# Kernel tuning notes

Measured on AMD Instinct MI355X. Metric: run time of the kernel, lower is better.

The kernel has to match this reference:

```python
import jax, jax.numpy as jnp
import numpy as np

N, EM, EW, L, S = 20000, 100000, 25000, 128, 6


def _mlp(x, W1, b1, W2, b2, g, beta):
    # Linear -> ReLU -> Linear -> LayerNorm
    h = jax.nn.relu(x @ W1 + b1) @ W2 + b2
    mu = jnp.mean(h, axis=-1, keepdims=True)
    var = jnp.mean((h - mu) ** 2, axis=-1, keepdims=True)
    return g * (h - mu) * jax.lax.rsqrt(var + 1e-5) + beta


def _scatter_mean(attr, recv, n):
    s = jax.ops.segment_sum(attr, recv, num_segments=n)
    c = jax.ops.segment_sum(jnp.ones((attr.shape[0], 1), attr.dtype), recv, num_segments=n)
    return s / jnp.maximum(c, 1.0)


def setup_inputs() -> dict:
    key = jax.random.key(0)
    ks = jax.random.split(key, 16)

    def w(k, shape, fan_in):
        return (jax.random.normal(k, shape, jnp.float32) / np.sqrt(fan_in).astype(np.float32))

    inp = {
        'x': jax.random.normal(ks[0], (N, L), jnp.float32),
        'mesh_edge_attr': jax.random.normal(ks[1], (EM, L), jnp.float32),
        'world_edge_attr': jax.random.normal(ks[2], (EW, L), jnp.float32),
        'mesh_edge_index': jax.random.randint(ks[3], (2, EM), 0, N),
        'world_edge_index': jax.random.randint(ks[4], (2, EW), 0, N),
    }
    i = 5
    for pre in ('me', 'we', 'nd'):
        inp[pre + '_W1'] = w(ks[i], (S, 3 * L, L), 3 * L); i += 1
        inp[pre + '_b1'] = jnp.zeros((S, L), jnp.float32)
        inp[pre + '_W2'] = w(ks[i], (S, L, L), L); i += 1
        inp[pre + '_b2'] = jnp.zeros((S, L), jnp.float32)
        inp[pre + '_g'] = jnp.ones((S, L), jnp.float32)
        inp[pre + '_beta'] = jnp.zeros((S, L), jnp.float32)
    return inp


def reference(x, mesh_edge_attr, world_edge_attr, mesh_edge_index, world_edge_index,
              me_W1, me_b1, me_W2, me_b2, me_g, me_beta,
              we_W1, we_b1, we_W2, we_b2, we_g, we_beta,
              nd_W1, nd_b1, nd_W2, nd_b2, nd_g, nd_beta):
    ms, mr = mesh_edge_index[0], mesh_edge_index[1]
    ws, wr = world_edge_index[0], world_edge_index[1]
    n = x.shape[0]

    def step(carry, p):
        x, mea, wea = carry
        (mW1, mb1, mW2, mb2, mg, mbe,
         wW1, wb1, wW2, wb2, wg, wbe,
         nW1, nb1, nW2, nb2, ng, nbe) = p
        # EdgeModel: gather + concat + MLP, residual into edge attrs
        mea = mea + _mlp(jnp.concatenate([x[ms], x[mr], mea], axis=-1), mW1, mb1, mW2, mb2, mg, mbe)
        wea = wea + _mlp(jnp.concatenate([x[ws], x[wr], wea], axis=-1), wW1, wb1, wW2, wb2, wg, wbe)
        # NodeModel: scatter-mean over both edge sets + concat + MLP, residual
        agg = jnp.concatenate([x, _scatter_mean(mea, mr, n), _scatter_mean(wea, wr, n)], axis=-1)
        x = x + _mlp(agg, nW1, nb1, nW2, nb2, ng, nbe)
        return (x, mea, wea), None

    params = (me_W1, me_b1, me_W2, me_b2, me_g, me_beta,
              we_W1, we_b1, we_W2, we_b2, we_g, we_beta,
              nd_W1, nd_b1, nd_W2, nd_b2, nd_g, nd_beta)
    (x, mea, wea), _ = jax.lax.scan(step, (x, mesh_edge_attr, world_edge_attr), params)
    return x, mea, wea
```

## Files before the change

### kernel.cpp

```cpp
#include <hip/hip_runtime.h>

constexpr int LDIM  = 128;
constexpr int NNODE = 20000;
constexpr int EM_N  = 100000;
constexpr int EW_N  = 25000;
constexpr int NSTEP = 6;

typedef short bf16x8 __attribute__((ext_vector_type(8)));
typedef short bf16x4 __attribute__((ext_vector_type(4)));
typedef float f32x4  __attribute__((ext_vector_type(4)));

struct MlpParams {
  const short* xb;
  const float* attrIn;
  float*       attrOut;
  short*       xbOut;
  const int*   src;
  const int*   dst;
  const int*   oidx;
  float*       origOut;
  const float* gsrc1;
  const float* gsrc2;
  const int*   off1;
  const int*   csr1;
  const int*   off2;
  const int*   csr2;
  const short* W1H;
  const short* W2H;
  const short* W2L;
  const float* b1;
  const float* b2;
  const float* gam;
  const float* bet;
  int nRows;
};

__device__ __forceinline__ short f2b(float f) {
  unsigned int u = __float_as_uint(f);
  u = (u + 0x7fffu + ((u >> 16) & 1u)) >> 16;
  return (short)u;
}
__device__ __forceinline__ float b2f(short s) {
  return __uint_as_float(((unsigned int)(unsigned short)s) << 16);
}
__device__ __forceinline__ bf16x4 cvt4(float4 a, float sc) {
  bf16x4 o;
  o[0] = f2b(a.x * sc); o[1] = f2b(a.y * sc);
  o[2] = f2b(a.z * sc); o[3] = f2b(a.w * sc);
  return o;
}
__device__ __forceinline__ bf16x4 cvt4v(f32x4 a, float sc) {
  bf16x4 o;
  o[0] = f2b(a[0] * sc); o[1] = f2b(a[1] * sc);
  o[2] = f2b(a[2] * sc); o[3] = f2b(a[3] * sc);
  return o;
}

__launch_bounds__(256, 2)
__global__ void edge_kernel(MlpParams pmA, MlpParams pmB, int blocksA) {
  const bool isA = (int)blockIdx.x < blocksA;
  const MlpParams P = isA ? pmA : pmB;
  const int bid  = isA ? (int)blockIdx.x : (int)blockIdx.x - blocksA;
  const int row0 = bid * 128;

  __shared__ __align__(16) short Abuf[128][40];
  __shared__ __align__(16) short Bhi[128][40];
  __shared__ __align__(16) short Blo[128][40];
  __shared__ __align__(16) short Hbuf[128][136];
  __shared__ float b1s[128], b2s[128], gs[128], bes[128];
  __shared__ int   idxa[128], idxb[128];
  __shared__ float sumL[2][128], sqL[2][128];
  __shared__ float muL[128], rsL[128];

  const int t = threadIdx.x;

  if (t < 128) {
    b1s[t] = P.b1[t];
    gs[t]  = P.gam[t];
    int r = row0 + t;
    idxa[t] = (r < P.nRows) ? P.src[r] : 0;
  } else {
    int t2 = t - 128;
    b2s[t2] = P.b2[t2];
    bes[t2] = P.bet[t2];
    int r = row0 + t2;
    idxb[t2] = (r < P.nRows) ? P.dst[r] : 0;
  }
  __syncthreads();

  const int l   = t & 63;
  const int wid = t >> 6;
  const int wr  = wid >> 1, wcc = wid & 1;
  const int lr  = l & 15,  lg  = l >> 4;

  const int  srow  = t >> 1, sh = t & 1;
  const int  sgRow = row0 + srow;
  const bool sval  = sgRow < P.nRows;
  const int  sgC   = sval ? sgRow : 0;
  const float vmask = sval ? 1.f : 0.f;

  const short* bx0   = P.xb + (size_t)idxa[srow] * LDIM + sh * 16;
  const short* bx1   = P.xb + (size_t)idxb[srow] * LDIM + sh * 16;
  const float* base2 = P.attrIn + (size_t)sgC * LDIM + sh * 16;

  const int wrow = t >> 1, wsh = t & 1;
  const short* w1base = P.W1H + (size_t)wrow * 384 + wsh * 16;

  f32x4 acc[4][4];
#pragma unroll
  for (int i = 0; i < 4; ++i)
#pragma unroll
    for (int j = 0; j < 4; ++j) acc[i][j] = f32x4{0.f, 0.f, 0.f, 0.f};

  const bf16x8 z8 = {0, 0, 0, 0, 0, 0, 0, 0};
  bf16x8 pB0, pB1;
  float4 pA0, pA1, pA2, pA3;
  bf16x8 pW0, pW1;
  {
    pB0 = *(const bf16x8*)bx0;
    pB1 = *(const bf16x8*)(bx0 + 8);
    pW0 = *(const bf16x8*)w1base;
    pW1 = *(const bf16x8*)(w1base + 8);
  }

#pragma unroll
  for (int kc = 0; kc < 12; ++kc) {
    const int seg = kc >> 2;
    if (kc > 0) __syncthreads();
    {
      if (seg < 2) {
        *(bf16x8*)&Abuf[srow][sh * 16]     = sval ? pB0 : z8;
        *(bf16x8*)&Abuf[srow][sh * 16 + 8] = sval ? pB1 : z8;
      } else {
        *(bf16x4*)&Abuf[srow][sh * 16 + 0]  = cvt4(pA0, vmask);
        *(bf16x4*)&Abuf[srow][sh * 16 + 4]  = cvt4(pA1, vmask);
        *(bf16x4*)&Abuf[srow][sh * 16 + 8]  = cvt4(pA2, vmask);
        *(bf16x4*)&Abuf[srow][sh * 16 + 12] = cvt4(pA3, vmask);
      }
      *(bf16x8*)&Bhi[wrow][wsh * 16]     = pW0;
      *(bf16x8*)&Bhi[wrow][wsh * 16 + 8] = pW1;
    }
    __syncthreads();
    if (kc < 11) {
      const int kn = kc + 1, segn = kn >> 2, partn = kn & 3;
      if (segn == 0) {
        pB0 = *(const bf16x8*)(bx0 + partn * 32);
        pB1 = *(const bf16x8*)(bx0 + partn * 32 + 8);
      } else if (segn == 1) {
        pB0 = *(const bf16x8*)(bx1 + partn * 32);
        pB1 = *(const bf16x8*)(bx1 + partn * 32 + 8);
      } else {
        const float4* bp = (const float4*)(base2 + partn * 32);
        pA0 = bp[0]; pA1 = bp[1]; pA2 = bp[2]; pA3 = bp[3];
      }
      pW0 = *(const bf16x8*)(w1base + kn * 32);
      pW1 = *(const bf16x8*)(w1base + kn * 32 + 8);
    }
    bf16x8 av[4], bh[4];
#pragma unroll
    for (int mi = 0; mi < 4; ++mi)
      av[mi] = *(const bf16x8*)&Abuf[wr * 64 + mi * 16 + lr][lg * 8];
#pragma unroll
    for (int ni = 0; ni < 4; ++ni)
      bh[ni] = *(const bf16x8*)&Bhi[wcc * 64 + ni * 16 + lr][lg * 8];
#pragma unroll
    for (int mi = 0; mi < 4; ++mi)
#pragma unroll
      for (int ni = 0; ni < 4; ++ni)
        acc[mi][ni] = __builtin_amdgcn_mfma_f32_16x16x32_bf16(av[mi], bh[ni], acc[mi][ni], 0, 0, 0);
  }

#pragma unroll
  for (int rt = 0; rt < 4; ++rt)
#pragma unroll
    for (int ct = 0; ct < 4; ++ct) {
      const int cc = wcc * 64 + ct * 16 + lr;
      const float bb = b1s[cc];
#pragma unroll
      for (int q = 0; q < 4; ++q) {
        const int rr = wr * 64 + rt * 16 + lg * 4 + q;
        Hbuf[rr][cc] = f2b(fmaxf(acc[rt][ct][q] + bb, 0.f));
      }
    }

  f32x4 acc2[4][4];
#pragma unroll
  for (int i = 0; i < 4; ++i)
#pragma unroll
    for (int j = 0; j < 4; ++j) acc2[i][j] = f32x4{0.f, 0.f, 0.f, 0.f};

  const short* w2hbase = P.W2H + (size_t)wrow * 128 + wsh * 16;
  const short* w2lbase = P.W2L + (size_t)wrow * 128 + wsh * 16;

  bf16x8 qh0 = *(const bf16x8*)w2hbase;
  bf16x8 qh1 = *(const bf16x8*)(w2hbase + 8);
  bf16x8 ql0 = *(const bf16x8*)w2lbase;
  bf16x8 ql1 = *(const bf16x8*)(w2lbase + 8);

#pragma unroll
  for (int kc = 0; kc < 4; ++kc) {
    __syncthreads();
    {
      *(bf16x8*)&Bhi[wrow][wsh * 16]     = qh0;
      *(bf16x8*)&Bhi[wrow][wsh * 16 + 8] = qh1;
      *(bf16x8*)&Blo[wrow][wsh * 16]     = ql0;
      *(bf16x8*)&Blo[wrow][wsh * 16 + 8] = ql1;
    }
    __syncthreads();
    if (kc < 3) {
      qh0 = *(const bf16x8*)(w2hbase + (kc + 1) * 32);
      qh1 = *(const bf16x8*)(w2hbase + (kc + 1) * 32 + 8);
      ql0 = *(const bf16x8*)(w2lbase + (kc + 1) * 32);
      ql1 = *(const bf16x8*)(w2lbase + (kc + 1) * 32 + 8);
    }
    bf16x8 av2[4], bh2[4], bl2[4];
#pragma unroll
    for (int rt = 0; rt < 4; ++rt)
      av2[rt] = *(const bf16x8*)&Hbuf[wr * 64 + rt * 16 + lr][kc * 32 + lg * 8];
#pragma unroll
    for (int ct = 0; ct < 4; ++ct) {
      bh2[ct] = *(const bf16x8*)&Bhi[wcc * 64 + ct * 16 + lr][lg * 8];
      bl2[ct] = *(const bf16x8*)&Blo[wcc * 64 + ct * 16 + lr][lg * 8];
    }
#pragma unroll
    for (int rt = 0; rt < 4; ++rt)
#pragma unroll
      for (int ct = 0; ct < 4; ++ct) {
        acc2[rt][ct] = __builtin_amdgcn_mfma_f32_16x16x32_bf16(av2[rt], bl2[ct], acc2[rt][ct], 0, 0, 0);
        acc2[rt][ct] = __builtin_amdgcn_mfma_f32_16x16x32_bf16(av2[rt], bh2[ct], acc2[rt][ct], 0, 0, 0);
      }
  }

  float s1[4][4], s2[4][4];
#pragma unroll
  for (int rt = 0; rt < 4; ++rt)
#pragma unroll
    for (int q = 0; q < 4; ++q) { s1[rt][q] = 0.f; s2[rt][q] = 0.f; }
#pragma unroll
  for (int rt = 0; rt < 4; ++rt)
#pragma unroll
    for (int ct = 0; ct < 4; ++ct) {
      const float bb = b2s[wcc * 64 + ct * 16 + lr];
#pragma unroll
      for (int q = 0; q < 4; ++q) {
        float v = acc2[rt][ct][q] + bb;
        acc2[rt][ct][q] = v;
        s1[rt][q] += v;
        s2[rt][q] += v * v;
      }
    }
#pragma unroll
  for (int m = 1; m < 16; m <<= 1) {
#pragma unroll
    for (int rt = 0; rt < 4; ++rt)
#pragma unroll
      for (int q = 0; q < 4; ++q) {
        s1[rt][q] += __shfl_xor(s1[rt][q], m);
        s2[rt][q] += __shfl_xor(s2[rt][q], m);
      }
  }
  __syncthreads();
  {
    const int rt = lr >> 2, q = lr & 3;
    const int rr = wr * 64 + rt * 16 + lg * 4 + q;
    sumL[wcc][rr] = s1[rt][q];
    sqL[wcc][rr]  = s2[rt][q];
  }
  __syncthreads();
  if (t < 128) {
    const float tot = sumL[0][t] + sumL[1][t];
    const float tsq = sqL[0][t] + sqL[1][t];
    const float mu  = tot * (1.0f / 128.0f);
    const float var = tsq * (1.0f / 128.0f) - mu * mu;
    muL[t] = mu;
    rsL[t] = rsqrtf(var + 1e-5f);
  }
  __syncthreads();

#pragma unroll
  for (int rt = 0; rt < 4; ++rt) {
#pragma unroll
    for (int q = 0; q < 4; ++q) {
      const int rr = wr * 64 + rt * 16 + lg * 4 + q;
      const int grow = row0 + rr;
      if (grow < P.nRows) {
        const float mu = muL[rr], rs = rsL[rr];
        const float* rin = P.attrIn + (size_t)grow * LDIM;
        float* rout = P.attrOut + (size_t)grow * LDIM;
        float* rout2 = nullptr;
        if (P.origOut) rout2 = P.origOut + (size_t)P.oidx[grow] * LDIM;
#pragma unroll
        for (int ct = 0; ct < 4; ++ct) {
          const int cc = wcc * 64 + ct * 16 + lr;
          const float o = gs[cc] * (acc2[rt][ct][q] - mu) * rs + bes[cc] + rin[cc];
          rout[cc] = o;
          if (rout2) rout2[cc] = o;
        }
      }
    }
  }
}

template<bool CONTIG>
__launch_bounds__(256, 3)
__global__ void node_kernel(MlpParams P) {
  constexpr int BR = 32;
  const int row0 = (int)blockIdx.x * BR;

  __shared__ __align__(16) short Abuf[BR][40];
  __shared__ __align__(16) short Bhi[128][40];
  __shared__ __align__(16) short Blo[128][40];
  __shared__ __align__(16) short Hbuf[BR][136];
  __shared__ float b1s[128], b2s[128], gs[128], bes[128];
  __shared__ float sumL[4][BR], sqL[4][BR], muL[BR], rsL[BR];

  const int t = threadIdx.x;
  if (t < 128) { b1s[t] = P.b1[t]; gs[t] = P.gam[t]; }
  else         { b2s[t - 128] = P.b2[t - 128]; bes[t - 128] = P.bet[t - 128]; }

  const int l  = t & 63;
  const int w  = t >> 6;
  const int lr = l & 15, lg = l >> 4;

  const int  srow  = t >> 3, sh = t & 7;
  const int  sgRow = row0 + srow;
  const bool sval  = sgRow < P.nRows;
  const int  sgC   = sval ? sgRow : 0;
  const int  myPart = sh >> 1, myHalf = sh & 1;

  const int wrow = t >> 1, wsh = t & 1;
  const short* w1base = P.W1H + (size_t)wrow * 384 + wsh * 16;
  const short* xrow   = P.xb + (size_t)sgC * LDIM + sh * 16;
  const bf16x8 z8 = {0, 0, 0, 0, 0, 0, 0, 0};

  f32x4 acc[2][2];
#pragma unroll
  for (int i = 0; i < 2; ++i)
#pragma unroll
    for (int j = 0; j < 2; ++j) acc[i][j] = f32x4{0.f, 0.f, 0.f, 0.f};

  f32x4 g[4];
#pragma unroll
  for (int j = 0; j < 4; ++j) g[j] = f32x4{0.f, 0.f, 0.f, 0.f};
  float scm = 1.f;
  {
    int beg = 0, end = 0;
    if (sval) { beg = P.off1[sgRow]; end = P.off1[sgRow + 1]; }
    for (int i = beg; i < end; ++i) {
      const size_t r = CONTIG ? (size_t)i : (size_t)P.csr1[i];
      const f32x4* p = (const f32x4*)(P.gsrc1 + r * LDIM + sh * 16);
#pragma unroll
      for (int j = 0; j < 4; ++j) g[j] += p[j];
    }
    scm = 1.0f / (float)max(end - beg, 1);
  }

  __syncthreads();

  float scw = 1.f;
#pragma unroll
  for (int kc = 0; kc < 12; ++kc) {
    const int seg = kc >> 2, part = kc & 3;
    if (kc > 0) __syncthreads();
    {
      if (myPart == part) {
        if (seg == 0) {
          const bf16x8* xp = (const bf16x8*)xrow;
          *(bf16x8*)&Abuf[srow][myHalf * 16]     = sval ? xp[0] : z8;
          *(bf16x8*)&Abuf[srow][myHalf * 16 + 8] = sval ? xp[1] : z8;
        } else {
          const float sc = (seg == 1) ? scm : scw;
          *(bf16x4*)&Abuf[srow][myHalf * 16 + 0]  = cvt4v(g[0], sc);
          *(bf16x4*)&Abuf[srow][myHalf * 16 + 4]  = cvt4v(g[1], sc);
          *(bf16x4*)&Abuf[srow][myHalf * 16 + 8]  = cvt4v(g[2], sc);
          *(bf16x4*)&Abuf[srow][myHalf * 16 + 12] = cvt4v(g[3], sc);
        }
      }
      const short* wsrc = w1base + kc * 32;
      *(bf16x8*)&Bhi[wrow][wsh * 16]     = *(const bf16x8*)wsrc;
      *(bf16x8*)&Bhi[wrow][wsh * 16 + 8] = *(const bf16x8*)(wsrc + 8);
      if (kc == 7) {
#pragma unroll
        for (int j = 0; j < 4; ++j) g[j] = f32x4{0.f, 0.f, 0.f, 0.f};
        int beg = 0, end = 0;
        if (sval) { beg = P.off2[sgRow]; end = P.off2[sgRow + 1]; }
        for (int i = beg; i < end; ++i) {
          const size_t r = CONTIG ? (size_t)i : (size_t)P.csr2[i];
          const f32x4* p = (const f32x4*)(P.gsrc2 + r * LDIM + sh * 16);
#pragma unroll
          for (int j = 0; j < 4; ++j) g[j] += p[j];
        }
        scw = 1.0f / (float)max(end - beg, 1);
      }
    }
    __syncthreads();
    bf16x8 av[2], bh[2];
#pragma unroll
    for (int mi = 0; mi < 2; ++mi)
      av[mi] = *(const bf16x8*)&Abuf[mi * 16 + lr][lg * 8];
#pragma unroll
    for (int ni = 0; ni < 2; ++ni)
      bh[ni] = *(const bf16x8*)&Bhi[w * 32 + ni * 16 + lr][lg * 8];
#pragma unroll
    for (int mi = 0; mi < 2; ++mi)
#pragma unroll
      for (int ni = 0; ni < 2; ++ni)
        acc[mi][ni] = __builtin_amdgcn_mfma_f32_16x16x32_bf16(av[mi], bh[ni], acc[mi][ni], 0, 0, 0);
  }

#pragma unroll
  for (int mi = 0; mi < 2; ++mi)
#pragma unroll
    for (int ni = 0; ni < 2; ++ni) {
      const int cc = w * 32 + ni * 16 + lr;
      const float bb = b1s[cc];
#pragma unroll
      for (int q = 0; q < 4; ++q) {
        const int rr = mi * 16 + lg * 4 + q;
        Hbuf[rr][cc] = f2b(fmaxf(acc[mi][ni][q] + bb, 0.f));
      }
    }

  f32x4 acc2[2][2];
#pragma unroll
  for (int i = 0; i < 2; ++i)
#pragma unroll
    for (int j = 0; j < 2; ++j) acc2[i][j] = f32x4{0.f, 0.f, 0.f, 0.f};

  const short* w2hbase = P.W2H + (size_t)wrow * 128 + wsh * 16;
  const short* w2lbase = P.W2L + (size_t)wrow * 128 + wsh * 16;
  bf16x8 qh0 = *(const bf16x8*)w2hbase;
  bf16x8 qh1 = *(const bf16x8*)(w2hbase + 8);
  bf16x8 ql0 = *(const bf16x8*)w2lbase;
  bf16x8 ql1 = *(const bf16x8*)(w2lbase + 8);

#pragma unroll
  for (int kc = 0; kc < 4; ++kc) {
    __syncthreads();
    {
      *(bf16x8*)&Bhi[wrow][wsh * 16]     = qh0;
      *(bf16x8*)&Bhi[wrow][wsh * 16 + 8] = qh1;
      *(bf16x8*)&Blo[wrow][wsh * 16]     = ql0;
      *(bf16x8*)&Blo[wrow][wsh * 16 + 8] = ql1;
    }
    __syncthreads();
    if (kc < 3) {
      qh0 = *(const bf16x8*)(w2hbase + (kc + 1) * 32);
      qh1 = *(const bf16x8*)(w2hbase + (kc + 1) * 32 + 8);
      ql0 = *(const bf16x8*)(w2lbase + (kc + 1) * 32);
      ql1 = *(const bf16x8*)(w2lbase + (kc + 1) * 32 + 8);
    }
    bf16x8 av2[2], bh2[2], bl2[2];
#pragma unroll
    for (int mi = 0; mi < 2; ++mi)
      av2[mi] = *(const bf16x8*)&Hbuf[mi * 16 + lr][kc * 32 + lg * 8];
#pragma unroll
    for (int ni = 0; ni < 2; ++ni) {
      bh2[ni] = *(const bf16x8*)&Bhi[w * 32 + ni * 16 + lr][lg * 8];
      bl2[ni] = *(const bf16x8*)&Blo[w * 32 + ni * 16 + lr][lg * 8];
    }
#pragma unroll
    for (int mi = 0; mi < 2; ++mi)
#pragma unroll
      for (int ni = 0; ni < 2; ++ni) {
        acc2[mi][ni] = __builtin_amdgcn_mfma_f32_16x16x32_bf16(av2[mi], bl2[ni], acc2[mi][ni], 0, 0, 0);
        acc2[mi][ni] = __builtin_amdgcn_mfma_f32_16x16x32_bf16(av2[mi], bh2[ni], acc2[mi][ni], 0, 0, 0);
      }
  }

  float s1[2][4], s2[2][4];
#pragma unroll
  for (int mi = 0; mi < 2; ++mi)
#pragma unroll
    for (int q = 0; q < 4; ++q) { s1[mi][q] = 0.f; s2[mi][q] = 0.f; }
#pragma unroll
  for (int mi = 0; mi < 2; ++mi)
#pragma unroll
    for (int ni = 0; ni < 2; ++ni) {
      const float bb = b2s[w * 32 + ni * 16 + lr];
#pragma unroll
      for (int q = 0; q < 4; ++q) {
        float v = acc2[mi][ni][q] + bb;
        acc2[mi][ni][q] = v;
        s1[mi][q] += v;
        s2[mi][q] += v * v;
      }
    }
#pragma unroll
  for (int m = 1; m < 16; m <<= 1) {
#pragma unroll
    for (int mi = 0; mi < 2; ++mi)
#pragma unroll
      for (int q = 0; q < 4; ++q) {
        s1[mi][q] += __shfl_xor(s1[mi][q], m);
        s2[mi][q] += __shfl_xor(s2[mi][q], m);
      }
  }
  __syncthreads();
  if (lr < 8) {
    const int mi = lr >> 2, q = lr & 3;
    const int rr = mi * 16 + lg * 4 + q;
    sumL[w][rr] = s1[mi][q];
    sqL[w][rr]  = s2[mi][q];
  }
  __syncthreads();
  if (t < BR) {
    float tot = 0.f, tsq = 0.f;
#pragma unroll
    for (int ww = 0; ww < 4; ++ww) { tot += sumL[ww][t]; tsq += sqL[ww][t]; }
    const float mu  = tot * (1.0f / 128.0f);
    const float var = tsq * (1.0f / 128.0f) - mu * mu;
    muL[t] = mu;
    rsL[t] = rsqrtf(var + 1e-5f);
  }
  __syncthreads();

#pragma unroll
  for (int mi = 0; mi < 2; ++mi) {
#pragma unroll
    for (int q = 0; q < 4; ++q) {
      const int rr = mi * 16 + lg * 4 + q;
      const int grow = row0 + rr;
      if (grow < P.nRows) {
        const float mu = muL[rr], rs = rsL[rr];
        const float* rin = P.attrIn + (size_t)grow * LDIM;
        float* rout = P.attrOut + (size_t)grow * LDIM;
        short* xbo  = P.xbOut + (size_t)grow * LDIM;
#pragma unroll
        for (int ni = 0; ni < 2; ++ni) {
          const int cc = w * 32 + ni * 16 + lr;
          const float o = gs[cc] * (acc2[mi][ni][q] - mu) * rs + bes[cc] + rin[cc];
          rout[cc] = o;
          xbo[cc] = f2b(o);
        }
      }
    }
  }
}

__global__ void prep_weights(const float* w1a, const float* w1b, const float* w1c,
                             const float* w2a, const float* w2b, const float* w2c,
                             short* w1h, short* w2h, short* w2l) {
  int i = blockIdx.x * 256 + threadIdx.x;
  constexpr int N1 = 18 * 128 * 384;
  constexpr int N2 = 18 * 128 * 128;
  if (i < N1) {
    int g = i / (128 * 384);
    int rem = i - g * (128 * 384);
    int n = rem / 384, k = rem - n * 384;
    int m = g / 6, s = g - m * 6;
    const float* src = (m == 0) ? w1a : (m == 1) ? w1b : w1c;
    w1h[i] = f2b(src[(size_t)s * (384 * 128) + (size_t)k * 128 + n]);
  } else if (i < N1 + N2) {
    int j = i - N1;
    int g = j / (128 * 128);
    int rem = j - g * (128 * 128);
    int n = rem / 128, k = rem - n * 128;
    int m = g / 6, s = g - m * 6;
    const float* src = (m == 0) ? w2a : (m == 1) ? w2b : w2c;
    float f = src[(size_t)s * (128 * 128) + (size_t)k * 128 + n];
    short hi = f2b(f);
    w2h[j] = hi;
    w2l[j] = f2b(f - b2f(hi));
  }
}

__global__ void prep_xb(const float* x, short* xb) {
  int i = blockIdx.x * 256 + threadIdx.x;
  if (i < NNODE * LDIM) xb[i] = f2b(x[i]);
}

__global__ void prep_deg(const int* mr, const int* wrcv, int* degm, int* degw) {
  int i = blockIdx.x * 256 + threadIdx.x;
  if (i < EM_N) atomicAdd(&degm[mr[i]], 1);
  else if (i < EM_N + EW_N) atomicAdd(&degw[wrcv[i - EM_N]], 1);
}

__global__ void prep_scan(const int* degm, const int* degw, int* moff, int* woff) {
  __shared__ int part[256];
  const int t = threadIdx.x;
  constexpr int NPT = (NNODE + 255) / 256;
#pragma unroll 1
  for (int pass = 0; pass < 2; ++pass) {
    const int* deg = pass == 0 ? degm : degw;
    int* off = pass == 0 ? moff : woff;
    int s = 0;
    for (int i = 0; i < NPT; ++i) {
      int n = t * NPT + i;
      if (n < NNODE) s += deg[n];
    }
    part[t] = s;
    __syncthreads();
    for (int d = 1; d < 256; d <<= 1) {
      int v = (t >= d) ? part[t - d] : 0;
      __syncthreads();
      part[t] += v;
      __syncthreads();
    }
    int base = (t == 0) ? 0 : part[t - 1];
    for (int i = 0; i < NPT; ++i) {
      int n = t * NPT + i;
      if (n < NNODE) { off[n] = base; base += deg[n]; }
    }
    if (t == 255) off[NNODE] = base;
    __syncthreads();
  }
}

__global__ void prep_fill(const int* ms, const int* mr, const int* wsnd, const int* wrcv,
                          const int* moff, const int* woff,
                          int* mcur, int* wcur, int* mcsr, int* wcsr,
                          int* psm, int* pdm, int* psw, int* pdw) {
  int i = blockIdx.x * 256 + threadIdx.x;
  if (i < EM_N) {
    int d = mr[i];
    int pos = moff[d] + atomicAdd(&mcur[d], 1);
    mcsr[pos] = i;
    psm[pos] = ms[i];
    pdm[pos] = d;
  } else if (i < EM_N + EW_N) {
    int j = i - EM_N;
    int d = wrcv[j];
    int pos = woff[d] + atomicAdd(&wcur[d], 1);
    wcsr[pos] = j;
    psw[pos] = wsnd[j];
    pdw[pos] = d;
  }
}

__global__ void prep_permute(const float* src_m, const float* src_w,
                             const int* mcsr, const int* wcsr,
                             float* dst_m, float* dst_w) {
  long i = (long)blockIdx.x * 256 + threadIdx.x;
  const long NM4 = (long)EM_N * 32, NW4 = (long)EW_N * 32;
  if (i < NM4) {
    long pos = i >> 5, c = i & 31;
    ((float4*)dst_m)[pos * 32 + c] = ((const float4*)src_m)[(size_t)mcsr[pos] * 32 + c];
  } else if (i < NM4 + NW4) {
    long j = i - NM4;
    long pos = j >> 5, c = j & 31;
    ((float4*)dst_w)[pos * 32 + c] = ((const float4*)src_w)[(size_t)wcsr[pos] * 32 + c];
  }
}

extern "C" void kernel_launch(void* const* d_in, const int* in_sizes, int n_in,
                              void* d_out, int out_size, void* d_ws, size_t ws_size,
                              hipStream_t stream) {
  (void)in_sizes; (void)n_in; (void)out_size;
  const float* x_in   = (const float*)d_in[0];
  const float* mea_in = (const float*)d_in[1];
  const float* wea_in = (const float*)d_in[2];
  const int*   mei    = (const int*)d_in[3];
  const int*   wei    = (const int*)d_in[4];
  const float* W1s[3] = { (const float*)d_in[5],  (const float*)d_in[11], (const float*)d_in[17] };
  const float* B1s[3] = { (const float*)d_in[6],  (const float*)d_in[12], (const float*)d_in[18] };
  const float* W2s[3] = { (const float*)d_in[7],  (const float*)d_in[13], (const float*)d_in[19] };
  const float* B2s[3] = { (const float*)d_in[8],  (const float*)d_in[14], (const float*)d_in[20] };
  const float* Gs[3]  = { (const float*)d_in[9],  (const float*)d_in[15], (const float*)d_in[21] };
  const float* Be[3]  = { (const float*)d_in[10], (const float*)d_in[16], (const float*)d_in[22] };

  float* xo  = (float*)d_out;
  float* meo = xo  + (size_t)NNODE * LDIM;
  float* weo = meo + (size_t)EM_N * LDIM;

  const size_t SORT_BYTES = ((size_t)EM_N + EW_N) * LDIM * 4;
  const size_t SMALL_BYTES = (size_t)20 * 1024 * 1024;
  const bool SORTED = ws_size >= SORT_BYTES + SMALL_BYTES;

  float* msort = (float*)d_ws;
  float* wsort = msort + (size_t)EM_N * LDIM;
  short* w1h = SORTED ? (short*)(wsort + (size_t)EW_N * LDIM) : (short*)d_ws;
  short* w2h = w1h + (size_t)18 * 128 * 384;
  short* w2l = w2h + (size_t)18 * 128 * 128;
  short* xb  = w2l + (size_t)18 * 128 * 128;
  int* degm = (int*)(xb + (size_t)NNODE * LDIM);
  int* degw = degm + NNODE;
  int* mcur = degw + NNODE;
  int* wcur = mcur + NNODE;
  int* moff = wcur + NNODE;
  int* woff = moff + (NNODE + 1);
  int* mcsr = woff + (NNODE + 1);
  int* wcsr = mcsr + EM_N;
  int* psm  = wcsr + EW_N;
  int* pdm  = psm + EM_N;
  int* psw  = pdm + EM_N;
  int* pdw  = psw + EW_N;

  hipMemsetAsync(degm, 0, (size_t)4 * NNODE * 4, stream);

  {
    int tot = 18 * 128 * 384 + 18 * 128 * 128;
    prep_weights<<<dim3((tot + 255) / 256), 256, 0, stream>>>(
        W1s[0], W1s[1], W1s[2], W2s[0], W2s[1], W2s[2], w1h, w2h, w2l);
  }
  prep_xb<<<dim3((NNODE * LDIM + 255) / 256), 256, 0, stream>>>(x_in, xb);
  prep_deg<<<dim3((EM_N + EW_N + 255) / 256), 256, 0, stream>>>(mei + EM_N, wei + EW_N, degm, degw);
  prep_scan<<<dim3(1), 256, 0, stream>>>(degm, degw, moff, woff);
  prep_fill<<<dim3((EM_N + EW_N + 255) / 256), 256, 0, stream>>>(
      mei, mei + EM_N, wei, wei + EW_N, moff, woff, mcur, wcur, mcsr, wcsr,
      psm, pdm, psw, pdw);
  if (SORTED) {
    long tot4 = ((long)EM_N + EW_N) * 32;
    prep_permute<<<dim3((unsigned)((tot4 + 255) / 256)), 256, 0, stream>>>(
        mea_in, wea_in, mcsr, wcsr, msort, wsort);
  }

  const int MB = (EM_N + 127) / 128;
  const int WB = (EW_N + 127) / 128;
  const int NB = (NNODE + 31) / 32;

  const float* mc = mea_in;
  const float* wc = wea_in;
  const float* xc = x_in;

  for (int s = 0; s < NSTEP; ++s) {
    MlpParams pm{}, pw{}, pn{};
    const bool last = (s == NSTEP - 1);

    pm.xb = xb;
    pm.W1H = w1h + (size_t)(0 * 6 + s) * 128 * 384;
    pm.W2H = w2h + (size_t)(0 * 6 + s) * 128 * 128;
    pm.W2L = w2l + (size_t)(0 * 6 + s) * 128 * 128;
    pm.b1 = B1s[0] + s * LDIM; pm.b2 = B2s[0] + s * LDIM;
    pm.gam = Gs[0] + s * LDIM; pm.bet = Be[0] + s * LDIM;
    pm.nRows = EM_N;

    pw.xb = xb;
    pw.W1H = w1h + (size_t)(1 * 6 + s) * 128 * 384;
    pw.W2H = w2h + (size_t)(1 * 6 + s) * 128 * 128;
    pw.W2L = w2l + (size_t)(1 * 6 + s) * 128 * 128;
    pw.b1 = B1s[1] + s * LDIM; pw.b2 = B2s[1] + s * LDIM;
    pw.gam = Gs[1] + s * LDIM; pw.bet = Be[1] + s * LDIM;
    pw.nRows = EW_N;

    if (SORTED) {
      pm.attrIn = msort; pm.attrOut = msort;
      pm.src = psm; pm.dst = pdm;
      pm.oidx = mcsr; pm.origOut = last ? meo : nullptr;
      pw.attrIn = wsort; pw.attrOut = wsort;
      pw.src = psw; pw.dst = pdw;
      pw.oidx = wcsr; pw.origOut = last ? weo : nullptr;
    } else {
      pm.attrIn = mc; pm.attrOut = meo;
      pm.src = mei; pm.dst = mei + EM_N;
      pw.attrIn = wc; pw.attrOut = weo;
      pw.src = wei; pw.dst = wei + EW_N;
    }

    edge_kernel<<<dim3(MB + WB), 256, 0, stream>>>(pm, pw, MB);

    pn.xb = xb; pn.attrIn = xc; pn.attrOut = xo; pn.xbOut = xb;
    pn.off1 = moff; pn.off2 = woff;
    pn.W1H = w1h + (size_t)(2 * 6 + s) * 128 * 384;
    pn.W2H = w2h + (size_t)(2 * 6 + s) * 128 * 128;
    pn.W2L = w2l + (size_t)(2 * 6 + s) * 128 * 128;
    pn.b1 = B1s[2] + s * LDIM; pn.b2 = B2s[2] + s * LDIM;
    pn.gam = Gs[2] + s * LDIM; pn.bet = Be[2] + s * LDIM;
    pn.nRows = NNODE;

    if (SORTED) {
      pn.gsrc1 = msort; pn.gsrc2 = wsort;
      node_kernel<true><<<dim3(NB), 256, 0, stream>>>(pn);
    } else {
      pn.gsrc1 = meo; pn.gsrc2 = weo;
      pn.csr1 = mcsr; pn.csr2 = wcsr;
      node_kernel<false><<<dim3(NB), 256, 0, stream>>>(pn);
    }

    mc = meo; wc = weo; xc = xo;
  }
}
```

Measured before the change: 805.7 us.

## Switch MFMA path to fp16, store edge attrs in fp16, drop W2 hi/lo split

Converts all bf16 operands to fp16 and uses the f16 MFMA. The persistent sorted edge-attribute buffers become fp16 instead of fp32, halving their traffic in the edge and node kernels. The second-layer weight is no longer split into hi/lo bf16 halves, removing half of the second GEMM's MFMAs and its LDS traffic. The unsorted fallback path is removed. In exchange, the residual edge state is accumulated in fp16 across steps, which risks precision loss and overflow.

```diff
diff --git a/kernel.cpp b/kernel.cpp
--- a/kernel.cpp
+++ b/kernel.cpp
@@ -6,28 +6,28 @@
 constexpr int EW_N  = 25000;
 constexpr int NSTEP = 6;
 
-typedef short bf16x8 __attribute__((ext_vector_type(8)));
-typedef short bf16x4 __attribute__((ext_vector_type(4)));
-typedef float f32x4  __attribute__((ext_vector_type(4)));
+typedef _Float16 f16;
+typedef _Float16 f16x8 __attribute__((ext_vector_type(8)));
+typedef _Float16 f16x4 __attribute__((ext_vector_type(4)));
+typedef float    f32x4 __attribute__((ext_vector_type(4)));
 
 struct MlpParams {
-  const short* xb;
-  const float* attrIn;
-  float*       attrOut;
-  short*       xbOut;
+  const f16*   xb;
+  const f16*   attrInH;
+  f16*         attrOutH;
+  const float* xIn;
+  float*       xOut;
+  f16*         xbOut;
   const int*   src;
   const int*   dst;
   const int*   oidx;
   float*       origOut;
-  const float* gsrc1;
-  const float* gsrc2;
+  const f16*   gsrc1;
+  const f16*   gsrc2;
   const int*   off1;
-  const int*   csr1;
   const int*   off2;
-  const int*   csr2;
-  const short* W1H;
-  const short* W2H;
-  const short* W2L;
+  const f16*   W1H;
+  const f16*   W2H;
   const float* b1;
   const float* b2;
   const float* gam;
@@ -35,24 +35,10 @@
   int nRows;
 };
 
-__device__ __forceinline__ short f2b(float f) {
-  unsigned int u = __float_as_uint(f);
-  u = (u + 0x7fffu + ((u >> 16) & 1u)) >> 16;
-  return (short)u;
-}
-__device__ __forceinline__ float b2f(short s) {
-  return __uint_as_float(((unsigned int)(unsigned short)s) << 16);
-}
-__device__ __forceinline__ bf16x4 cvt4(float4 a, float sc) {
-  bf16x4 o;
-  o[0] = f2b(a.x * sc); o[1] = f2b(a.y * sc);
-  o[2] = f2b(a.z * sc); o[3] = f2b(a.w * sc);
-  return o;
-}
-__device__ __forceinline__ bf16x4 cvt4v(f32x4 a, float sc) {
-  bf16x4 o;
-  o[0] = f2b(a[0] * sc); o[1] = f2b(a[1] * sc);
-  o[2] = f2b(a[2] * sc); o[3] = f2b(a[3] * sc);
+__device__ __forceinline__ f16x4 cvt4h(f32x4 a, float sc) {
+  f16x4 o;
+  o[0] = (f16)(a[0] * sc); o[1] = (f16)(a[1] * sc);
+  o[2] = (f16)(a[2] * sc); o[3] = (f16)(a[3] * sc);
   return o;
 }
 
@@ -63,10 +49,9 @@
   const int bid  = isA ? (int)blockIdx.x : (int)blockIdx.x - blocksA;
   const int row0 = bid * 128;
 
-  __shared__ __align__(16) short Abuf[128][40];
-  __shared__ __align__(16) short Bhi[128][40];
-  __shared__ __align__(16) short Blo[128][40];
-  __shared__ __align__(16) short Hbuf[128][136];
+  __shared__ __align__(16) f16 Abuf[128][40];
+  __shared__ __align__(16) f16 Bhi[128][40];
+  __shared__ __align__(16) f16 Hbuf[128][136];
   __shared__ float b1s[128], b2s[128], gs[128], bes[128];
   __shared__ int   idxa[128], idxb[128];
   __shared__ float sumL[2][128], sqL[2][128];
@@ -97,14 +82,13 @@
   const int  sgRow = row0 + srow;
   const bool sval  = sgRow < P.nRows;
   const int  sgC   = sval ? sgRow : 0;
-  const float vmask = sval ? 1.f : 0.f;
-
-  const short* bx0   = P.xb + (size_t)idxa[srow] * LDIM + sh * 16;
-  const short* bx1   = P.xb + (size_t)idxb[srow] * LDIM + sh * 16;
-  const float* base2 = P.attrIn + (size_t)sgC * LDIM + sh * 16;
+
+  const f16* bx0 = P.xb + (size_t)idxa[srow] * LDIM + sh * 16;
+  const f16* bx1 = P.xb + (size_t)idxb[srow] * LDIM + sh * 16;
+  const f16* bx2 = P.attrInH + (size_t)sgC * LDIM + sh * 16;
 
   const int wrow = t >> 1, wsh = t & 1;
-  const short* w1base = P.W1H + (size_t)wrow * 384 + wsh * 16;
+  const f16* w1base = P.W1H + (size_t)wrow * 384 + wsh * 16;
 
   f32x4 acc[4][4];
 #pragma unroll
@@ -112,62 +96,45 @@
 #pragma unroll
     for (int j = 0; j < 4; ++j) acc[i][j] = f32x4{0.f, 0.f, 0.f, 0.f};
 
-  const bf16x8 z8 = {0, 0, 0, 0, 0, 0, 0, 0};
-  bf16x8 pB0, pB1;
-  float4 pA0, pA1, pA2, pA3;
-  bf16x8 pW0, pW1;
+  const f16x8 z8 = {0, 0, 0, 0, 0, 0, 0, 0};
+  f16x8 pB0, pB1, pW0, pW1;
   {
-    pB0 = *(const bf16x8*)bx0;
-    pB1 = *(const bf16x8*)(bx0 + 8);
-    pW0 = *(const bf16x8*)w1base;
-    pW1 = *(const bf16x8*)(w1base + 8);
+    pB0 = *(const f16x8*)bx0;
+    pB1 = *(const f16x8*)(bx0 + 8);
+    pW0 = *(const f16x8*)w1base;
+    pW1 = *(const f16x8*)(w1base + 8);
   }
 
 #pragma unroll
   for (int kc = 0; kc < 12; ++kc) {
-    const int seg = kc >> 2;
     if (kc > 0) __syncthreads();
     {
-      if (seg < 2) {
-        *(bf16x8*)&Abuf[srow][sh * 16]     = sval ? pB0 : z8;
-        *(bf16x8*)&Abuf[srow][sh * 16 + 8] = sval ? pB1 : z8;
-      } else {
-        *(bf16x4*)&Abuf[srow][sh * 16 + 0]  = cvt4(pA0, vmask);
-        *(bf16x4*)&Abuf[srow][sh * 16 + 4]  = cvt4(pA1, vmask);
-        *(bf16x4*)&Abuf[srow][sh * 16 + 8]  = cvt4(pA2, vmask);
-        *(bf16x4*)&Abuf[srow][sh * 16 + 12] = cvt4(pA3, vmask);
-      }
-      *(bf16x8*)&Bhi[wrow][wsh * 16]     = pW0;
-      *(bf16x8*)&Bhi[wrow][wsh * 16 + 8] = pW1;
+      *(f16x8*)&Abuf[srow][sh * 16]     = sval ? pB0 : z8;
+      *(f16x8*)&Abuf[srow][sh * 16 + 8] = sval ? pB1 : z8;
+      *(f16x8*)&Bhi[wrow][wsh * 16]     = pW0;
+      *(f16x8*)&Bhi[wrow][wsh * 16 + 8] = pW1;
     }
     __syncthreads();
     if (kc < 11) {
       const int kn = kc + 1, segn = kn >> 2, partn = kn & 3;
-      if (segn == 0) {
-        pB0 = *(const bf16x8*)(bx0 + partn * 32);
-        pB1 = *(const bf16x8*)(bx0 + partn * 32 + 8);
-      } else if (segn == 1) {
-        pB0 = *(const bf16x8*)(bx1 + partn * 32);
-        pB1 = *(const bf16x8*)(bx1 + partn * 32 + 8);
-      } else {
-        const float4* bp = (const float4*)(base2 + partn * 32);
-        pA0 = bp[0]; pA1 = bp[1]; pA2 = bp[2]; pA3 = bp[3];
-      }
-      pW0 = *(const bf16x8*)(w1base + kn * 32);
-      pW1 = *(const bf16x8*)(w1base + kn * 32 + 8);
-    }
-    bf16x8 av[4], bh[4];
+      const f16* bp = (segn == 0 ? bx0 : segn == 1 ? bx1 : bx2) + partn * 32;
+      pB0 = *(const f16x8*)bp;
+      pB1 = *(const f16x8*)(bp + 8);
+      pW0 = *(const f16x8*)(w1base + kn * 32);
+      pW1 = *(const f16x8*)(w1base + kn * 32 + 8);
+    }
+    f16x8 av[4], bh[4];
 #pragma unroll
     for (int mi = 0; mi < 4; ++mi)
-      av[mi] = *(const bf16x8*)&Abuf[wr * 64 + mi * 16 + lr][lg * 8];
+      av[mi] = *(const f16x8*)&Abuf[wr * 64 + mi * 16 + lr][lg * 8];
 #pragma unroll
     for (int ni = 0; ni < 4; ++ni)
-      bh[ni] = *(const bf16x8*)&Bhi[wcc * 64 + ni * 16 + lr][lg * 8];
+      bh[ni] = *(const f16x8*)&Bhi[wcc * 64 + ni * 16 + lr][lg * 8];
 #pragma unroll
     for (int mi = 0; mi < 4; ++mi)
 #pragma unroll
       for (int ni = 0; ni < 4; ++ni)
-        acc[mi][ni] = __builtin_amdgcn_mfma_f32_16x16x32_bf16(av[mi], bh[ni], acc[mi][ni], 0, 0, 0);
+        acc[mi][ni] = __builtin_amdgcn_mfma_f32_16x16x32_f16(av[mi], bh[ni], acc[mi][ni], 0, 0, 0);
   }
 
 #pragma unroll
@@ -179,7 +146,7 @@
 #pragma unroll
       for (int q = 0; q < 4; ++q) {
         const int rr = wr * 64 + rt * 16 + lg * 4 + q;
-        Hbuf[rr][cc] = f2b(fmaxf(acc[rt][ct][q] + bb, 0.f));
+        Hbuf[rr][cc] = (f16)fmaxf(acc[rt][ct][q] + bb, 0.f);
       }
     }
 
@@ -189,46 +156,34 @@
 #pragma unroll
     for (int j = 0; j < 4; ++j) acc2[i][j] = f32x4{0.f, 0.f, 0.f, 0.f};
 
-  const short* w2hbase = P.W2H + (size_t)wrow * 128 + wsh * 16;
-  const short* w2lbase = P.W2L + (size_t)wrow * 128 + wsh * 16;
-
-  bf16x8 qh0 = *(const bf16x8*)w2hbase;
-  bf16x8 qh1 = *(const bf16x8*)(w2hbase + 8);
-  bf16x8 ql0 = *(const bf16x8*)w2lbase;
-  bf16x8 ql1 = *(const bf16x8*)(w2lbase + 8);
+  const f16* w2base = P.W2H + (size_t)wrow * 128 + wsh * 16;
+  f16x8 q0 = *(const f16x8*)w2base;
+  f16x8 q1 = *(const f16x8*)(w2base + 8);
 
 #pragma unroll
   for (int kc = 0; kc < 4; ++kc) {
     __syncthreads();
     {
-      *(bf16x8*)&Bhi[wrow][wsh * 16]     = qh0;
-      *(bf16x8*)&Bhi[wrow][wsh * 16 + 8] = qh1;
-      *(bf16x8*)&Blo[wrow][wsh * 16]     = ql0;
-      *(bf16x8*)&Blo[wrow][wsh * 16 + 8] = ql1;
+      *(f16x8*)&Bhi[wrow][wsh * 16]     = q0;
+      *(f16x8*)&Bhi[wrow][wsh * 16 + 8] = q1;
     }
     __syncthreads();
     if (kc < 3) {
-      qh0 = *(const bf16x8*)(w2hbase + (kc + 1) * 32);
-      qh1 = *(const bf16x8*)(w2hbase + (kc + 1) * 32 + 8);
-      ql0 = *(const bf16x8*)(w2lbase + (kc + 1) * 32);
-      ql1 = *(const bf16x8*)(w2lbase + (kc + 1) * 32 + 8);
-    }
-    bf16x8 av2[4], bh2[4], bl2[4];
+      q0 = *(const f16x8*)(w2base + (kc + 1) * 32);
+      q1 = *(const f16x8*)(w2base + (kc + 1) * 32 + 8);
+    }
+    f16x8 av2[4], bh2[4];
 #pragma unroll
     for (int rt = 0; rt < 4; ++rt)
-      av2[rt] = *(const bf16x8*)&Hbuf[wr * 64 + rt * 16 + lr][kc * 32 + lg * 8];
-#pragma unroll
-    for (int ct = 0; ct < 4; ++ct) {
-      bh2[ct] = *(const bf16x8*)&Bhi[wcc * 64 + ct * 16 + lr][lg * 8];
-      bl2[ct] = *(const bf16x8*)&Blo[wcc * 64 + ct * 16 + lr][lg * 8];
-    }
+      av2[rt] = *(const f16x8*)&Hbuf[wr * 64 + rt * 16 + lr][kc * 32 + lg * 8];
+#pragma unroll
+    for (int ct = 0; ct < 4; ++ct)
+      bh2[ct] = *(const f16x8*)&Bhi[wcc * 64 + ct * 16 + lr][lg * 8];
 #pragma unroll
     for (int rt = 0; rt < 4; ++rt)
 #pragma unroll
-      for (int ct = 0; ct < 4; ++ct) {
-        acc2[rt][ct] = __builtin_amdgcn_mfma_f32_16x16x32_bf16(av2[rt], bl2[ct], acc2[rt][ct], 0, 0, 0);
-        acc2[rt][ct] = __builtin_amdgcn_mfma_f32_16x16x32_bf16(av2[rt], bh2[ct], acc2[rt][ct], 0, 0, 0);
-      }
+      for (int ct = 0; ct < 4; ++ct)
+        acc2[rt][ct] = __builtin_amdgcn_mfma_f32_16x16x32_f16(av2[rt], bh2[ct], acc2[rt][ct], 0, 0, 0);
   }
 
   float s1[4][4], s2[4][4];
@@ -285,15 +240,15 @@
       const int grow = row0 + rr;
       if (grow < P.nRows) {
         const float mu = muL[rr], rs = rsL[rr];
-        const float* rin = P.attrIn + (size_t)grow * LDIM;
-        float* rout = P.attrOut + (size_t)grow * LDIM;
+        const f16* rin = P.attrInH + (size_t)grow * LDIM;
+        f16* rout = P.attrOutH + (size_t)grow * LDIM;
         float* rout2 = nullptr;
         if (P.origOut) rout2 = P.origOut + (size_t)P.oidx[grow] * LDIM;
 #pragma unroll
         for (int ct = 0; ct < 4; ++ct) {
           const int cc = wcc * 64 + ct * 16 + lr;
-          const float o = gs[cc] * (acc2[rt][ct][q] - mu) * rs + bes[cc] + rin[cc];
-          rout[cc] = o;
+          const float o = gs[cc] * (acc2[rt][ct][q] - mu) * rs + bes[cc] + (float)rin[cc];
+          rout[cc] = (f16)o;
           if (rout2) rout2[cc] = o;
         }
       }
@@ -301,16 +256,14 @@
   }
 }
 
-template<bool CONTIG>
 __launch_bounds__(256, 3)
 __global__ void node_kernel(MlpParams P) {
   constexpr int BR = 32;
   const int row0 = (int)blockIdx.x * BR;
 
-  __shared__ __align__(16) short Abuf[BR][40];
-  __shared__ __align__(16) short Bhi[128][40];
-  __shared__ __align__(16) short Blo[128][40];
-  __shared__ __align__(16) short Hbuf[BR][136];
+  __shared__ __align__(16) f16 Abuf[BR][40];
+  __shared__ __align__(16) f16 Bhi[128][40];
+  __shared__ __align__(16) f16 Hbuf[BR][136];
   __shared__ float b1s[128], b2s[128], gs[128], bes[128];
   __shared__ float sumL[4][BR], sqL[4][BR], muL[BR], rsL[BR];
 
@@ -329,9 +282,9 @@
   const int  myPart = sh >> 1, myHalf = sh & 1;
 
   const int wrow = t >> 1, wsh = t & 1;
-  const short* w1base = P.W1H + (size_t)wrow * 384 + wsh * 16;
-  const short* xrow   = P.xb + (size_t)sgC * LDIM + sh * 16;
-  const bf16x8 z8 = {0, 0, 0, 0, 0, 0, 0, 0};
+  const f16* w1base = P.W1H + (size_t)wrow * 384 + wsh * 16;
+  const f16* xrow   = P.xb + (size_t)sgC * LDIM + sh * 16;
+  const f16x8 z8 = {0, 0, 0, 0, 0, 0, 0, 0};
 
   f32x4 acc[2][2];
 #pragma unroll
@@ -347,10 +300,14 @@
     int beg = 0, end = 0;
     if (sval) { beg = P.off1[sgRow]; end = P.off1[sgRow + 1]; }
     for (int i = beg; i < end; ++i) {
-      const size_t r = CONTIG ? (size_t)i : (size_t)P.csr1[i];
-      const f32x4* p = (const f32x4*)(P.gsrc1 + r * LDIM + sh * 16);
-#pragma unroll
-      for (int j = 0; j < 4; ++j) g[j] += p[j];
+      const f16* er = P.gsrc1 + (size_t)i * LDIM + sh * 16;
+      const f16x8 v0 = *(const f16x8*)er;
+      const f16x8 v1 = *(const f16x8*)(er + 8);
+#pragma unroll
+      for (int e = 0; e < 8; ++e) {
+        g[e >> 2][e & 3]       += (float)v0[e];
+        g[2 + (e >> 2)][e & 3] += (float)v1[e];
+      }
     }
     scm = 1.0f / (float)max(end - beg, 1);
   }
@@ -365,47 +322,51 @@
     {
       if (myPart == part) {
         if (seg == 0) {
-          const bf16x8* xp = (const bf16x8*)xrow;
-          *(bf16x8*)&Abuf[srow][myHalf * 16]     = sval ? xp[0] : z8;
-          *(bf16x8*)&Abuf[srow][myHalf * 16 + 8] = sval ? xp[1] : z8;
+          const f16x8* xp = (const f16x8*)xrow;
+          *(f16x8*)&Abuf[srow][myHalf * 16]     = sval ? xp[0] : z8;
+          *(f16x8*)&Abuf[srow][myHalf * 16 + 8] = sval ? xp[1] : z8;
         } else {
           const float sc = (seg == 1) ? scm : scw;
-          *(bf16x4*)&Abuf[srow][myHalf * 16 + 0]  = cvt4v(g[0], sc);
-          *(bf16x4*)&Abuf[srow][myHalf * 16 + 4]  = cvt4v(g[1], sc);
-          *(bf16x4*)&Abuf[srow][myHalf * 16 + 8]  = cvt4v(g[2], sc);
-          *(bf16x4*)&Abuf[srow][myHalf * 16 + 12] = cvt4v(g[3], sc);
+          *(f16x4*)&Abuf[srow][myHalf * 16 + 0]  = cvt4h(g[0], sc);
+          *(f16x4*)&Abuf[srow][myHalf * 16 + 4]  = cvt4h(g[1], sc);
+          *(f16x4*)&Abuf[srow][myHalf * 16 + 8]  = cvt4h(g[2], sc);
+          *(f16x4*)&Abuf[srow][myHalf * 16 + 12] = cvt4h(g[3], sc);
         }
       }
-      const short* wsrc = w1base + kc * 32;
-      *(bf16x8*)&Bhi[wrow][wsh * 16]     = *(const bf16x8*)wsrc;
-      *(bf16x8*)&Bhi[wrow][wsh * 16 + 8] = *(const bf16x8*)(wsrc + 8);
+      const f16* wsrc = w1base + kc * 32;
+      *(f16x8*)&Bhi[wrow][wsh * 16]     = *(const f16x8*)wsrc;
+      *(f16x8*)&Bhi[wrow][wsh * 16 + 8] = *(const f16x8*)(wsrc + 8);
       if (kc == 7) {
 #pragma unroll
         for (int j = 0; j < 4; ++j) g[j] = f32x4{0.f, 0.f, 0.f, 0.f};
         int beg = 0, end = 0;
         if (sval) { beg = P.off2[sgRow]; end = P.off2[sgRow + 1]; }
         for (int i = beg; i < end; ++i) {
-          const size_t r = CONTIG ? (size_t)i : (size_t)P.csr2[i];
-          const f32x4* p = (const f32x4*)(P.gsrc2 + r * LDIM + sh * 16);
-#pragma unroll
-          for (int j = 0; j < 4; ++j) g[j] += p[j];
+          const f16* er = P.gsrc2 + (size_t)i * LDIM + sh * 16;
+          const f16x8 v0 = *(const f16x8*)er;
+          const f16x8 v1 = *(const f16x8*)(er + 8);
+#pragma unroll
+          for (int e = 0; e < 8; ++e) {
+            g[e >> 2][e & 3]       += (float)v0[e];
+            g[2 + (e >> 2)][e & 3] += (float)v1[e];
+          }
         }
         scw = 1.0f / (float)max(end - beg, 1);
       }
     }
     __syncthreads();
-    bf16x8 av[2], bh[2];
+    f16x8 av[2], bh[2];
 #pragma unroll
     for (int mi = 0; mi < 2; ++mi)
-      av[mi] = *(const bf16x8*)&Abuf[mi * 16 + lr][lg * 8];
+      av[mi] = *(const f16x8*)&Abuf[mi * 16 + lr][lg * 8];
 #pragma unroll
     for (int ni = 0; ni < 2; ++ni)
-      bh[ni] = *(const bf16x8*)&Bhi[w * 32 + ni * 16 + lr][lg * 8];
+      bh[ni] = *(const f16x8*)&Bhi[w * 32 + ni * 16 + lr][lg * 8];
 #pragma unroll
     for (int mi = 0; mi < 2; ++mi)
 #pragma unroll
       for (int ni = 0; ni < 2; ++ni)
-        acc[mi][ni] = __builtin_amdgcn_mfma_f32_16x16x32_bf16(av[mi], bh[ni], acc[mi][ni], 0, 0, 0);
+        acc[mi][ni] = __builtin_amdgcn_mfma_f32_16x16x32_f16(av[mi], bh[ni], acc[mi][ni], 0, 0, 0);
   }
 
 #pragma unroll
@@ -417,7 +378,7 @@
 #pragma unroll
       for (int q = 0; q < 4; ++q) {
         const int rr = mi * 16 + lg * 4 + q;
-        Hbuf[rr][cc] = f2b(fmaxf(acc[mi][ni][q] + bb, 0.f));
+        Hbuf[rr][cc] = (f16)fmaxf(acc[mi][ni][q] + bb, 0.f);
       }
     }
 
@@ -427,45 +388,34 @@
 #pragma unroll
     for (int j = 0; j < 2; ++j) acc2[i][j] = f32x4{0.f, 0.f, 0.f, 0.f};
 
-  const short* w2hbase = P.W2H + (size_t)wrow * 128 + wsh * 16;
-  const short* w2lbase = P.W2L + (size_t)wrow * 128 + wsh * 16;
-  bf16x8 qh0 = *(const bf16x8*)w2hbase;
-  bf16x8 qh1 = *(const bf16x8*)(w2hbase + 8);
-  bf16x8 ql0 = *(const bf16x8*)w2lbase;
-  bf16x8 ql1 = *(const bf16x8*)(w2lbase + 8);
+  const f16* w2base = P.W2H + (size_t)wrow * 128 + wsh * 16;
+  f16x8 q0 = *(const f16x8*)w2base;
+  f16x8 q1 = *(const f16x8*)(w2base + 8);
 
 #pragma unroll
   for (int kc = 0; kc < 4; ++kc) {
     __syncthreads();
     {
-      *(bf16x8*)&Bhi[wrow][wsh * 16]     = qh0;
-      *(bf16x8*)&Bhi[wrow][wsh * 16 + 8] = qh1;
-      *(bf16x8*)&Blo[wrow][wsh * 16]     = ql0;
-      *(bf16x8*)&Blo[wrow][wsh * 16 + 8] = ql1;
+      *(f16x8*)&Bhi[wrow][wsh * 16]     = q0;
+      *(f16x8*)&Bhi[wrow][wsh * 16 + 8] = q1;
     }
     __syncthreads();
     if (kc < 3) {
-      qh0 = *(const bf16x8*)(w2hbase + (kc + 1) * 32);
-      qh1 = *(const bf16x8*)(w2hbase + (kc + 1) * 32 + 8);
-      ql0 = *(const bf16x8*)(w2lbase + (kc + 1) * 32);
-      ql1 = *(const bf16x8*)(w2lbase + (kc + 1) * 32 + 8);
-    }
-    bf16x8 av2[2], bh2[2], bl2[2];
+      q0 = *(const f16x8*)(w2base + (kc + 1) * 32);
+      q1 = *(const f16x8*)(w2base + (kc + 1) * 32 + 8);
+    }
+    f16x8 av2[2], bh2[2];
 #pragma unroll
     for (int mi = 0; mi < 2; ++mi)
-      av2[mi] = *(const bf16x8*)&Hbuf[mi * 16 + lr][kc * 32 + lg * 8];
-#pragma unroll
-    for (int ni = 0; ni < 2; ++ni) {
-      bh2[ni] = *(const bf16x8*)&Bhi[w * 32 + ni * 16 + lr][lg * 8];
-      bl2[ni] = *(const bf16x8*)&Blo[w * 32 + ni * 16 + lr][lg * 8];
-    }
+      av2[mi] = *(const f16x8*)&Hbuf[mi * 16 + lr][kc * 32 + lg * 8];
+#pragma unroll
+    for (int ni = 0; ni < 2; ++ni)
+      bh2[ni] = *(const f16x8*)&Bhi[w * 32 + ni * 16 + lr][lg * 8];
 #pragma unroll
     for (int mi = 0; mi < 2; ++mi)
 #pragma unroll
-      for (int ni = 0; ni < 2; ++ni) {
-        acc2[mi][ni] = __builtin_amdgcn_mfma_f32_16x16x32_bf16(av2[mi], bl2[ni], acc2[mi][ni], 0, 0, 0);
-        acc2[mi][ni] = __builtin_amdgcn_mfma_f32_16x16x32_bf16(av2[mi], bh2[ni], acc2[mi][ni], 0, 0, 0);
-      }
+      for (int ni = 0; ni < 2; ++ni)
+        acc2[mi][ni] = __builtin_amdgcn_mfma_f32_16x16x32_f16(av2[mi], bh2[ni], acc2[mi][ni], 0, 0, 0);
   }
 
   float s1[2][4], s2[2][4];
@@ -523,15 +473,15 @@
       const int grow = row0 + rr;
       if (grow < P.nRows) {
         const float mu = muL[rr], rs = rsL[rr];
-        const float* rin = P.attrIn + (size_t)grow * LDIM;
-        float* rout = P.attrOut + (size_t)grow * LDIM;
-        short* xbo  = P.xbOut + (size_t)grow * LDIM;
+        const float* rin = P.xIn + (size_t)grow * LDIM;
+        float* rout = P.xOut + (size_t)grow * LDIM;
+        f16* xbo = P.xbOut + (size_t)grow * LDIM;
 #pragma unroll
         for (int ni = 0; ni < 2; ++ni) {
           const int cc = w * 32 + ni * 16 + lr;
           const float o = gs[cc] * (acc2[mi][ni][q] - mu) * rs + bes[cc] + rin[cc];
           rout[cc] = o;
-          xbo[cc] = f2b(o);
+          xbo[cc] = (f16)o;
         }
       }
     }
@@ -540,7 +490,7 @@
 
 __global__ void prep_weights(const float* w1a, const float* w1b, const float* w1c,
                              const float* w2a, const float* w2b, const float* w2c,
-                             short* w1h, short* w2h, short* w2l) {
+                             f16* w1h, f16* w2h) {
   int i = blockIdx.x * 256 + threadIdx.x;
   constexpr int N1 = 18 * 128 * 384;
   constexpr int N2 = 18 * 128 * 128;
@@ -550,7 +500,7 @@
     int n = rem / 384, k = rem - n * 384;
     int m = g / 6, s = g - m * 6;
     const float* src = (m == 0) ? w1a : (m == 1) ? w1b : w1c;
-    w1h[i] = f2b(src[(size_t)s * (384 * 128) + (size_t)k * 128 + n]);
+    w1h[i] = (f16)src[(size_t)s * (384 * 128) + (size_t)k * 128 + n];
   } else if (i < N1 + N2) {
     int j = i - N1;
     int g = j / (128 * 128);
@@ -558,16 +508,13 @@
     int n = rem / 128, k = rem - n * 128;
     int m = g / 6, s = g - m * 6;
     const float* src = (m == 0) ? w2a : (m == 1) ? w2b : w2c;
-    float f = src[(size_t)s * (128 * 128) + (size_t)k * 128 + n];
-    short hi = f2b(f);
-    w2h[j] = hi;
-    w2l[j] = f2b(f - b2f(hi));
-  }
-}
-
-__global__ void prep_xb(const float* x, short* xb) {
+    w2h[j] = (f16)src[(size_t)s * (128 * 128) + (size_t)k * 128 + n];
+  }
+}
+
+__global__ void prep_xb(const float* x, f16* xb) {
   int i = blockIdx.x * 256 + threadIdx.x;
-  if (i < NNODE * LDIM) xb[i] = f2b(x[i]);
+  if (i < NNODE * LDIM) xb[i] = (f16)x[i];
 }
 
 __global__ void prep_deg(const int* mr, const int* wrcv, int* degm, int* degw) {
@@ -630,23 +577,31 @@
 
 __global__ void prep_permute(const float* src_m, const float* src_w,
                              const int* mcsr, const int* wcsr,
-                             float* dst_m, float* dst_w) {
+                             f16* dst_m, f16* dst_w) {
   long i = (long)blockIdx.x * 256 + threadIdx.x;
-  const long NM4 = (long)EM_N * 32, NW4 = (long)EW_N * 32;
-  if (i < NM4) {
-    long pos = i >> 5, c = i & 31;
-    ((float4*)dst_m)[pos * 32 + c] = ((const float4*)src_m)[(size_t)mcsr[pos] * 32 + c];
-  } else if (i < NM4 + NW4) {
-    long j = i - NM4;
-    long pos = j >> 5, c = j & 31;
-    ((float4*)dst_w)[pos * 32 + c] = ((const float4*)src_w)[(size_t)wcsr[pos] * 32 + c];
+  const long NM8 = (long)EM_N * 16, NW8 = (long)EW_N * 16;
+  if (i < NM8) {
+    long pos = i >> 4, c = (i & 15) * 8;
+    const float* s = src_m + (size_t)mcsr[pos] * LDIM + c;
+    f16x8 o;
+#pragma unroll
+    for (int e = 0; e < 8; ++e) o[e] = (f16)s[e];
+    *(f16x8*)(dst_m + pos * LDIM + c) = o;
+  } else if (i < NM8 + NW8) {
+    long j = i - NM8;
+    long pos = j >> 4, c = (j & 15) * 8;
+    const float* s = src_w + (size_t)wcsr[pos] * LDIM + c;
+    f16x8 o;
+#pragma unroll
+    for (int e = 0; e < 8; ++e) o[e] = (f16)s[e];
+    *(f16x8*)(dst_w + pos * LDIM + c) = o;
   }
 }
 
 extern "C" void kernel_launch(void* const* d_in, const int* in_sizes, int n_in,
                               void* d_out, int out_size, void* d_ws, size_t ws_size,
                               hipStream_t stream) {
-  (void)in_sizes; (void)n_in; (void)out_size;
+  (void)in_sizes; (void)n_in; (void)out_size; (void)ws_size;
   const float* x_in   = (const float*)d_in[0];
   const float* mea_in = (const float*)d_in[1];
   const float* wea_in = (const float*)d_in[2];
@@ -663,35 +618,30 @@
   float* meo = xo  + (size_t)NNODE * LDIM;
   float* weo = meo + (size_t)EM_N * LDIM;
 
-  const size_t SORT_BYTES = ((size_t)EM_N + EW_N) * LDIM * 4;
-  const size_t SMALL_BYTES = (size_t)20 * 1024 * 1024;
-  const bool SORTED = ws_size >= SORT_BYTES + SMALL_BYTES;
-
-  float* msort = (float*)d_ws;
-  float* wsort = msort + (size_t)EM_N * LDIM;
-  short* w1h = SORTED ? (short*)(wsort + (size_t)EW_N * LDIM) : (short*)d_ws;
-  short* w2h = w1h + (size_t)18 * 128 * 384;
-  short* w2l = w2h + (size_t)18 * 128 * 128;
-  short* xb  = w2l + (size_t)18 * 128 * 128;
-  int* degm = (int*)(xb + (size_t)NNODE * LDIM);
-  int* degw = degm + NNODE;
-  int* mcur = degw + NNODE;
-  int* wcur = mcur + NNODE;
-  int* moff = wcur + NNODE;
-  int* woff = moff + (NNODE + 1);
-  int* mcsr = woff + (NNODE + 1);
-  int* wcsr = mcsr + EM_N;
-  int* psm  = wcsr + EW_N;
-  int* pdm  = psm + EM_N;
-  int* psw  = pdm + EM_N;
-  int* pdw  = psw + EW_N;
+  f16* msort = (f16*)d_ws;
+  f16* wsort = msort + (size_t)EM_N * LDIM;
+  f16* w1h   = wsort + (size_t)EW_N * LDIM;
+  f16* w2h   = w1h + (size_t)18 * 128 * 384;
+  f16* xb    = w2h + (size_t)18 * 128 * 128;
+  int* degm  = (int*)(xb + (size_t)NNODE * LDIM);
+  int* degw  = degm + NNODE;
+  int* mcur  = degw + NNODE;
+  int* wcur  = mcur + NNODE;
+  int* moff  = wcur + NNODE;
+  int* woff  = moff + (NNODE + 1);
+  int* mcsr  = woff + (NNODE + 1);
+  int* wcsr  = mcsr + EM_N;
+  int* psm   = wcsr + EW_N;
+  int* pdm   = psm + EM_N;
+  int* psw   = pdm + EM_N;
+  int* pdw   = psw + EW_N;
 
   hipMemsetAsync(degm, 0, (size_t)4 * NNODE * 4, stream);
 
   {
     int tot = 18 * 128 * 384 + 18 * 128 * 128;
     prep_weights<<<dim3((tot + 255) / 256), 256, 0, stream>>>(
-        W1s[0], W1s[1], W1s[2], W2s[0], W2s[1], W2s[2], w1h, w2h, w2l);
+        W1s[0], W1s[1], W1s[2], W2s[0], W2s[1], W2s[2], w1h, w2h);
   }
   prep_xb<<<dim3((NNODE * LDIM + 255) / 256), 256, 0, stream>>>(x_in, xb);
   prep_deg<<<dim3((EM_N + EW_N + 255) / 256), 256, 0, stream>>>(mei + EM_N, wei + EW_N, degm, degw);
@@ -699,9 +649,9 @@
   prep_fill<<<dim3((EM_N + EW_N + 255) / 256), 256, 0, stream>>>(
       mei, mei + EM_N, wei, wei + EW_N, moff, woff, mcur, wcur, mcsr, wcsr,
       psm, pdm, psw, pdw);
-  if (SORTED) {
-    long tot4 = ((long)EM_N + EW_N) * 32;
-    prep_permute<<<dim3((unsigned)((tot4 + 255) / 256)), 256, 0, stream>>>(
+  {
+    long tot8 = ((long)EM_N + EW_N) * 16;
+    prep_permute<<<dim3((unsigned)((tot8 + 255) / 256)), 256, 0, stream>>>(
         mea_in, wea_in, mcsr, wcsr, msort, wsort);
   }
 
@@ -709,8 +659,6 @@
   const int WB = (EW_N + 127) / 128;
   const int NB = (NNODE + 31) / 32;
 
-  const float* mc = mea_in;
-  const float* wc = wea_in;
   const float* xc = x_in;
 
   for (int s = 0; s < NSTEP; ++s) {
@@ -718,55 +666,38 @@
     const bool last = (s == NSTEP - 1);
 
     pm.xb = xb;
+    pm.attrInH = msort; pm.attrOutH = msort;
+    pm.src = psm; pm.dst = pdm;
+    pm.oidx = mcsr; pm.origOut = last ? meo : nullptr;
     pm.W1H = w1h + (size_t)(0 * 6 + s) * 128 * 384;
     pm.W2H = w2h + (size_t)(0 * 6 + s) * 128 * 128;
-    pm.W2L = w2l + (size_t)(0 * 6 + s) * 128 * 128;
     pm.b1 = B1s[0] + s * LDIM; pm.b2 = B2s[0] + s * LDIM;
     pm.gam = Gs[0] + s * LDIM; pm.bet = Be[0] + s * LDIM;
     pm.nRows = EM_N;
 
     pw.xb = xb;
+    pw.attrInH = wsort; pw.attrOutH = wsort;
+    pw.src = psw; pw.dst = pdw;
+    pw.oidx = wcsr; pw.origOut = last ? weo : nullptr;
     pw.W1H = w1h + (size_t)(1 * 6 + s) * 128 * 384;
     pw.W2H = w2h + (size_t)(1 * 6 + s) * 128 * 128;
-    pw.W2L = w2l + (size_t)(1 * 6 + s) * 128 * 128;
     pw.b1 = B1s[1] + s * LDIM; pw.b2 = B2s[1] + s * LDIM;
     pw.gam = Gs[1] + s * LDIM; pw.bet = Be[1] + s * LDIM;
     pw.nRows = EW_N;
 
-    if (SORTED) {
-      pm.attrIn = msort; pm.attrOut = msort;
-      pm.src = psm; pm.dst = pdm;
-      pm.oidx = mcsr; pm.origOut = last ? meo : nullptr;
-      pw.attrIn = wsort; pw.attrOut = wsort;
-      pw.src = psw; pw.dst = pdw;
-      pw.oidx = wcsr; pw.origOut = last ? weo : nullptr;
-    } else {
-      pm.attrIn = mc; pm.attrOut = meo;
-      pm.src = mei; pm.dst = mei + EM_N;
-      pw.attrIn = wc; pw.attrOut = weo;
-      pw.src = wei; pw.dst = wei + EW_N;
-    }
-
     edge_kernel<<<dim3(MB + WB), 256, 0, stream>>>(pm, pw, MB);
 
-    pn.xb = xb; pn.attrIn = xc; pn.attrOut = xo; pn.xbOut = xb;
+    pn.xb = xb; pn.xIn = xc; pn.xOut = xo; pn.xbOut = xb;
+    pn.gsrc1 = msort; pn.gsrc2 = wsort;
     pn.off1 = moff; pn.off2 = woff;
     pn.W1H = w1h + (size_t)(2 * 6 + s) * 128 * 384;
     pn.W2H = w2h + (size_t)(2 * 6 + s) * 128 * 128;
-    pn.W2L = w2l + (size_t)(2 * 6 + s) * 128 * 128;
     pn.b1 = B1s[2] + s * LDIM; pn.b2 = B2s[2] + s * LDIM;
     pn.gam = Gs[2] + s * LDIM; pn.bet = Be[2] + s * LDIM;
     pn.nRows = NNODE;
 
-    if (SORTED) {
-      pn.gsrc1 = msort; pn.gsrc2 = wsort;
-      node_kernel<true><<<dim3(NB), 256, 0, stream>>>(pn);
-    } else {
-      pn.gsrc1 = meo; pn.gsrc2 = weo;
-      pn.csr1 = mcsr; pn.csr2 = wcsr;
-      node_kernel<false><<<dim3(NB), 256, 0, stream>>>(pn);
-    }
-
-    mc = meo; wc = weo; xc = xo;
-  }
-}
+    node_kernel<<<dim3(NB), 256, 0, stream>>>(pn);
+
+    xc = xo;
+  }
+}
```

Result: slower. 823.1 us (+2.2%).
